# Kernel optimization log

Measured on AMD Instinct MI355X. Metric: run time of the kernel, lower is better.

The kernel has to match this reference:

```python
import jax, jax.numpy as jnp
import numpy as np

N = 50000
E = 800000
IN_DIM = 128
OUT_DIM = 128
FEAT_DIM = 64  # dstfeat_fc is nn.Linear(64, out_dim) in the source


def setup_inputs() -> dict:
    key = jax.random.key(0)
    k = jax.random.split(key, 6)
    h = jax.random.normal(k[0], (N, IN_DIM), dtype=jnp.float32)
    feat = jax.random.normal(k[1], (N, FEAT_DIM), dtype=jnp.float32)
    W_fc = jax.random.normal(k[2], (IN_DIM, OUT_DIM), dtype=jnp.float32) / np.sqrt(IN_DIM)
    W_dst = jax.random.normal(k[3], (FEAT_DIM, OUT_DIM), dtype=jnp.float32) / np.sqrt(FEAT_DIM)
    src = jax.random.randint(k[4], (E,), 0, N, dtype=jnp.int64 if jax.config.jax_enable_x64 else jnp.int32)
    dst = jax.random.randint(k[5], (E,), 0, N, dtype=jnp.int64 if jax.config.jax_enable_x64 else jnp.int32)
    return {"h": h, "feat": feat, "W_fc": W_fc, "W_dst": W_dst, "src": src, "dst": dst}


def reference(h, feat, W_fc, W_dst, src, dst):
    # z = fc(h)  -- per-node linear (bias-free)
    z = h @ W_fc                      # [N, D]
    # dstfeat = dstfeat_fc(feat) -- computed per-edge in DGL, per-node here (same math)
    dz = feat @ W_dst                 # [N, D]
    # edge_attention: e_ij = <z_src, dstfeat_dst>
    e = jnp.sum(z[src] * dz[dst], axis=-1)          # [E]
    # reduce_func: softmax over each destination's incoming mailbox, numerically stable
    emax = jax.ops.segment_max(e, dst, num_segments=N)
    emax = jnp.where(jnp.isfinite(emax), emax, 0.0)  # nodes with no in-edges
    ex = jnp.exp(e - emax[dst])                      # [E]
    denom = jax.ops.segment_sum(ex, dst, num_segments=N)
    alpha = ex / jnp.where(denom == 0, 1.0, denom)[dst]
    # weighted sum of source messages z into destination nodes
    out = jax.ops.segment_sum(alpha[:, None] * z[src], dst, num_segments=N)  # [N, D]
    return out
```

## Files before the change

kernel.cpp:

```cpp
#include <hip/hip_runtime.h>
#include <hip/hip_fp16.h>
#include <math.h>

#define IN_DIM   128
#define OUT_DIM  128
#define FEAT_DIM 64
#define NB       64
#define EBUF     6144

typedef _Float16 h2v __attribute__((ext_vector_type(2)));

__device__ __forceinline__ float2 h2f2(unsigned u) {
    __half2 h = *reinterpret_cast<const __half2*>(&u);
    return __half22float2(h);
}
__device__ __forceinline__ unsigned f2h2(float a, float b) {
    __half2 h = __floats2half2_rn(a, b);
    return *reinterpret_cast<unsigned*>(&h);
}
__device__ __forceinline__ float dot2(unsigned a, unsigned b, float c) {
#if __has_builtin(__builtin_amdgcn_fdot2)
    return __builtin_amdgcn_fdot2(*reinterpret_cast<h2v*>(&a),
                                  *reinterpret_cast<h2v*>(&b), c, false);
#else
    float2 fa = h2f2(a), fb = h2f2(b);
    return c + fa.x * fb.x + fa.y * fb.y;
#endif
}

__global__ __launch_bounds__(256) void k_wt(const float* __restrict__ Wfc,
                                            const float* __restrict__ Wdst,
                                            unsigned* __restrict__ Wfp,
                                            unsigned* __restrict__ Wdp,
                                            unsigned* __restrict__ bcounts) {
    int idx = blockIdx.x * 256 + threadIdx.x;
    if (idx < 8192) {
        int k2 = idx >> 7, c = idx & 127;
        Wfp[idx] = f2h2(Wfc[(2 * k2) * 128 + c], Wfc[(2 * k2 + 1) * 128 + c]);
    } else if (idx < 12288) {
        int i2 = idx - 8192;
        int k2 = i2 >> 7, c = i2 & 127;
        Wdp[i2] = f2h2(Wdst[(2 * k2) * 128 + c], Wdst[(2 * k2 + 1) * 128 + c]);
    }
    if (idx < 256) bcounts[idx] = 0u;
}

__global__ __launch_bounds__(256) void k_linear(
        const float* __restrict__ h, const float* __restrict__ feat,
        const unsigned* __restrict__ Wfp, const unsigned* __restrict__ Wdp,
        unsigned short* __restrict__ z_h, unsigned short* __restrict__ dz_h,
        int N, int nbz) {
    int t  = threadIdx.x;
    int c  = t & 31;
    int j0 = t >> 5;
    int b  = blockIdx.x;
    bool do_z = (b < nbz);
    int n0 = (do_z ? b : b - nbz) * NB;

    __shared__ uint2 sh[NB * 32];

    float4 acc[8];
#pragma unroll
    for (int jj = 0; jj < 8; ++jj) acc[jj] = make_float4(0.f, 0.f, 0.f, 0.f);

    if (do_z) {
        for (int i = t; i < NB * 32; i += 256) {
            int row = i >> 5, col = i & 31;
            int n = min(n0 + row, N - 1);
            float4 v = ((const float4*)(h + (size_t)n * IN_DIM))[col];
            sh[i] = make_uint2(f2h2(v.x, v.y), f2h2(v.z, v.w));
        }
        __syncthreads();

        const uint4* Wp4 = (const uint4*)Wfp;
#pragma unroll 2
        for (int k4 = 0; k4 < 32; ++k4) {
            uint4 wA = Wp4[(size_t)(2 * k4) * 32 + c];
            uint4 wB = Wp4[(size_t)(2 * k4 + 1) * 32 + c];
#pragma unroll
            for (int jj = 0; jj < 8; ++jj) {
                uint2 q = sh[(j0 * 8 + jj) * 32 + k4];
                acc[jj].x = dot2(q.y, wB.x, dot2(q.x, wA.x, acc[jj].x));
                acc[jj].y = dot2(q.y, wB.y, dot2(q.x, wA.y, acc[jj].y));
                acc[jj].z = dot2(q.y, wB.z, dot2(q.x, wA.z, acc[jj].z));
                acc[jj].w = dot2(q.y, wB.w, dot2(q.x, wA.w, acc[jj].w));
            }
        }
#pragma unroll
        for (int jj = 0; jj < 8; ++jj) {
            int n = n0 + j0 * 8 + jj;
            if (n < N) {
                uint2 pk = make_uint2(f2h2(acc[jj].x, acc[jj].y),
                                      f2h2(acc[jj].z, acc[jj].w));
                ((uint2*)(z_h + (size_t)n * OUT_DIM))[c] = pk;
            }
        }
    } else {
        for (int i = t; i < NB * 16; i += 256) {
            int row = i >> 4, col = i & 15;
            int n = min(n0 + row, N - 1);
            float4 v = ((const float4*)(feat + (size_t)n * FEAT_DIM))[col];
            sh[i] = make_uint2(f2h2(v.x, v.y), f2h2(v.z, v.w));
        }
        __syncthreads();

        const uint4* Wd4 = (const uint4*)Wdp;
#pragma unroll 2
        for (int k4 = 0; k4 < 16; ++k4) {
            uint4 wA = Wd4[(size_t)(2 * k4) * 32 + c];
            uint4 wB = Wd4[(size_t)(2 * k4 + 1) * 32 + c];
#pragma unroll
            for (int jj = 0; jj < 8; ++jj) {
                uint2 q = sh[(j0 * 8 + jj) * 16 + k4];
                acc[jj].x = dot2(q.y, wB.x, dot2(q.x, wA.x, acc[jj].x));
                acc[jj].y = dot2(q.y, wB.y, dot2(q.x, wA.y, acc[jj].y));
                acc[jj].z = dot2(q.y, wB.z, dot2(q.x, wA.z, acc[jj].z));
                acc[jj].w = dot2(q.y, wB.w, dot2(q.x, wA.w, acc[jj].w));
            }
        }
#pragma unroll
        for (int jj = 0; jj < 8; ++jj) {
            int n = n0 + j0 * 8 + jj;
            if (n < N) {
                uint2 pk = make_uint2(f2h2(acc[jj].x, acc[jj].y),
                                      f2h2(acc[jj].z, acc[jj].w));
                ((uint2*)(dz_h + (size_t)n * OUT_DIM))[c] = pk;
            }
        }
    }
}

__global__ __launch_bounds__(256) void k_bhist(const int* __restrict__ dst,
                                               unsigned* __restrict__ bcounts,
                                               int E, int nbkt) {
    __shared__ unsigned hist[256];
    int t = threadIdx.x;
    hist[t] = 0;
    __syncthreads();
    for (int i = blockIdx.x * 256 + t; i < E; i += gridDim.x * 256)
        atomicAdd(&hist[dst[i] >> 8], 1u);
    __syncthreads();
    if (t < nbkt && hist[t]) atomicAdd(&bcounts[t], hist[t]);
}

__global__ __launch_bounds__(256) void k_bscan(const unsigned* __restrict__ bcounts,
                                               unsigned* __restrict__ bstart,
                                               unsigned* __restrict__ bcursor, int nbkt) {
    __shared__ unsigned s[256];
    int t = threadIdx.x;
    unsigned v = (t < nbkt) ? bcounts[t] : 0u;
    s[t] = v;
    __syncthreads();
    for (int off = 1; off < 256; off <<= 1) {
        unsigned u = (t >= off) ? s[t - off] : 0u;
        __syncthreads();
        s[t] += u;
        __syncthreads();
    }
    if (t < nbkt) {
        unsigned excl = s[t] - v;
        bstart[t]  = excl;
        bcursor[t] = excl;
        if (t == nbkt - 1) bstart[nbkt] = s[t];
    }
}

__global__ __launch_bounds__(256) void k_bin(
        const int* __restrict__ dst, const int* __restrict__ src,
        unsigned* __restrict__ bcursor, unsigned* __restrict__ binned,
        int E, int nbkt) {
    __shared__ unsigned hist[256];
    __shared__ unsigned base[256];
    __shared__ unsigned cur[256];
    int t = threadIdx.x;
    int per = (E + gridDim.x - 1) / gridDim.x;
    int lo = blockIdx.x * per;
    int hi = min(E, lo + per);

    hist[t] = 0;
    cur[t]  = 0;
    __syncthreads();
    for (int i = lo + t; i < hi; i += 256)
        atomicAdd(&hist[dst[i] >> 8], 1u);
    __syncthreads();
    if (t < nbkt && hist[t]) base[t] = atomicAdd(&bcursor[t], hist[t]);
    __syncthreads();
    for (int i = lo + t; i < hi; i += 256) {
        int d = dst[i];
        int bk = d >> 8;
        unsigned slot = base[bk] + atomicAdd(&cur[bk], 1u);
        binned[slot] = (unsigned)src[i] | ((unsigned)(d & 255) << 24);
    }
}

__global__ __launch_bounds__(256) void k_sortx(
        const unsigned* __restrict__ binned, const unsigned* __restrict__ bstart,
        unsigned* __restrict__ offsets, unsigned* __restrict__ csr,
        int N, int E, int nbkt) {
    __shared__ unsigned ebuf[EBUF];
    __shared__ unsigned lhist[256];
    __shared__ unsigned loffx[256];
    __shared__ unsigned lcur[256];
    int b = blockIdx.x, t = threadIdx.x;
    unsigned lo = bstart[b], hi = bstart[b + 1];
    int cnt = (int)(hi - lo);
    int d0 = b << 8;
    int nd = min(N - d0, 256);
    bool fits = (cnt <= EBUF);

    lhist[t] = 0;
    lcur[t]  = 0;
    __syncthreads();

    if (fits) {
        for (int i = t; i < cnt; i += 256) {
            unsigned e = binned[lo + i];
            ebuf[i] = e;
            atomicAdd(&lhist[e >> 24], 1u);
        }
    } else {
        for (int i = t; i < cnt; i += 256)
            atomicAdd(&lhist[binned[lo + i] >> 24], 1u);
    }
    __syncthreads();

    unsigned v = lhist[t];
    loffx[t] = v;
    __syncthreads();
    for (int off = 1; off < 256; off <<= 1) {
        unsigned u = (t >= off) ? loffx[t - off] : 0u;
        __syncthreads();
        loffx[t] += u;
        __syncthreads();
    }
    unsigned excl = loffx[t] - v;
    __syncthreads();
    loffx[t] = excl;
    __syncthreads();

    if (t < nd) offsets[d0 + t] = lo + excl;
    if (b == nbkt - 1 && t == 0) offsets[N] = (unsigned)E;

    if (fits) {
        for (int i = t; i < cnt; i += 256) {
            unsigned e = ebuf[i];
            int ld = (int)(e >> 24);
            unsigned pos = loffx[ld] + atomicAdd(&lcur[ld], 1u);
            csr[lo + pos] = e & 0xFFFFFFu;
        }
    } else {
        for (int i = t; i < cnt; i += 256) {
            unsigned e = binned[lo + i];
            int ld = (int)(e >> 24);
            unsigned pos = loffx[ld] + atomicAdd(&lcur[ld], 1u);
            csr[lo + pos] = e & 0xFFFFFFu;
        }
    }
}

__global__ __launch_bounds__(256) void k_node(
        const unsigned short* __restrict__ z_h, const unsigned short* __restrict__ dz_h,
        const unsigned* __restrict__ offsets, const unsigned* __restrict__ csr,
        float* __restrict__ out, int N) {
    int lane = threadIdx.x & 63;
    int wv   = threadIdx.x >> 6;
    int g    = lane >> 4;
    int l16  = lane & 15;
    int n = blockIdx.x * 4 + wv;
    if (n >= N) return;

    unsigned start = offsets[n];
    int deg = (int)(offsets[n + 1] - start);
    float4* orow = (float4*)(out + (size_t)n * OUT_DIM);
    if (deg == 0) {
        if (g == 0) {
            orow[2 * l16]     = make_float4(0.f, 0.f, 0.f, 0.f);
            orow[2 * l16 + 1] = make_float4(0.f, 0.f, 0.f, 0.f);
        }
        return;
    }

    uint4 dq = ((const uint4*)(dz_h + (size_t)n * OUT_DIM))[l16];

    float a[8];
#pragma unroll
    for (int k = 0; k < 8; ++k) a[k] = 0.f;
    float denom = 0.f;

    for (int i = 0; i < deg; i += 8) {
        int eA = i + g;
        int eB = i + 4 + g;
        bool vA = eA < deg;
        bool vB = eB < deg;
        int sA = vA ? (int)csr[start + eA] : 0;
        int sB = vB ? (int)csr[start + eB] : 0;
        uint4 qA = ((const uint4*)(z_h + (size_t)sA * OUT_DIM))[l16];
        uint4 qB = ((const uint4*)(z_h + (size_t)sB * OUT_DIM))[l16];

        float pA = dot2(qA.w, dq.w, dot2(qA.z, dq.z, dot2(qA.y, dq.y, dot2(qA.x, dq.x, 0.f))));
        float pB = dot2(qB.w, dq.w, dot2(qB.z, dq.z, dot2(qB.y, dq.y, dot2(qB.x, dq.x, 0.f))));
#pragma unroll
        for (int off = 1; off <= 8; off <<= 1) {
            pA += __shfl_xor(pA, off);
            pB += __shfl_xor(pB, off);
        }
        float wA = vA ? __expf(pA) : 0.f;
        float wB = vB ? __expf(pB) : 0.f;
        denom += wA + wB;

        float2 zA01 = h2f2(qA.x), zA23 = h2f2(qA.y), zA45 = h2f2(qA.z), zA67 = h2f2(qA.w);
        float2 zB01 = h2f2(qB.x), zB23 = h2f2(qB.y), zB45 = h2f2(qB.z), zB67 = h2f2(qB.w);
        a[0] += wA * zA01.x + wB * zB01.x;  a[1] += wA * zA01.y + wB * zB01.y;
        a[2] += wA * zA23.x + wB * zB23.x;  a[3] += wA * zA23.y + wB * zB23.y;
        a[4] += wA * zA45.x + wB * zB45.x;  a[5] += wA * zA45.y + wB * zB45.y;
        a[6] += wA * zA67.x + wB * zB67.x;  a[7] += wA * zA67.y + wB * zB67.y;
    }

#pragma unroll
    for (int off = 16; off <= 32; off <<= 1) {
#pragma unroll
        for (int k = 0; k < 8; ++k) a[k] += __shfl_xor(a[k], off);
        denom += __shfl_xor(denom, off);
    }

    if (g == 0) {
        float inv = 1.f / denom;
        orow[2 * l16]     = make_float4(a[0] * inv, a[1] * inv, a[2] * inv, a[3] * inv);
        orow[2 * l16 + 1] = make_float4(a[4] * inv, a[5] * inv, a[6] * inv, a[7] * inv);
    }
}

extern "C" void kernel_launch(void* const* d_in, const int* in_sizes, int n_in,
                              void* d_out, int out_size, void* d_ws, size_t ws_size,
                              hipStream_t stream) {
    const float* h    = (const float*)d_in[0];
    const float* feat = (const float*)d_in[1];
    const float* Wfc  = (const float*)d_in[2];
    const float* Wdst = (const float*)d_in[3];
    const int*   src  = (const int*)d_in[4];
    const int*   dst  = (const int*)d_in[5];
    float*       out  = (float*)d_out;

    int N = in_sizes[0] / IN_DIM;
    int E = in_sizes[4];

    char* ws = (char*)d_ws;
    unsigned short* z_h  = (unsigned short*)ws; ws += (size_t)N * OUT_DIM * sizeof(unsigned short);
    unsigned short* dz_h = (unsigned short*)ws; ws += (size_t)N * OUT_DIM * sizeof(unsigned short);
    unsigned* Wfp      = (unsigned*)ws; ws += (size_t)8192 * sizeof(unsigned);
    unsigned* Wdp      = (unsigned*)ws; ws += (size_t)4096 * sizeof(unsigned);
    unsigned* binned   = (unsigned*)ws; ws += (size_t)E * sizeof(unsigned);
    unsigned* bcounts  = (unsigned*)ws; ws += (size_t)256 * sizeof(unsigned);
    unsigned* bstart   = (unsigned*)ws; ws += (size_t)260 * sizeof(unsigned);
    unsigned* bcursor  = (unsigned*)ws; ws += (size_t)256 * sizeof(unsigned);
    unsigned* offsets  = (unsigned*)ws; ws += (size_t)(N + 1) * sizeof(unsigned);
    unsigned* csr      = (unsigned*)ws;

    int nbz  = (N + NB - 1) / NB;
    int nbkt = (N + 255) / 256;

    k_wt     <<<48, 256, 0, stream>>>(Wfc, Wdst, Wfp, Wdp, bcounts);
    k_linear <<<2 * nbz, 256, 0, stream>>>(h, feat, Wfp, Wdp, z_h, dz_h, N, nbz);
    k_bhist  <<<512, 256, 0, stream>>>(dst, bcounts, E, nbkt);
    k_bscan  <<<1, 256, 0, stream>>>(bcounts, bstart, bcursor, nbkt);
    k_bin    <<<512, 256, 0, stream>>>(dst, src, bcursor, binned, E, nbkt);
    k_sortx  <<<nbkt, 256, 0, stream>>>(binned, bstart, offsets, csr, N, E, nbkt);
    k_node   <<<(N + 3) / 4, 256, 0, stream>>>(z_h, dz_h, offsets, csr, out, N);
}
```

Before: 123.4 us.

## Fold histogram into linear kernel and recompute bucket scan per block

```diff
diff --git a/kernel.cpp b/kernel.cpp
--- a/kernel.cpp
+++ b/kernel.cpp
@@ -6,6 +6,7 @@
 #define OUT_DIM  128
 #define FEAT_DIM 64
 #define NB       64
+#define NHB      512
 #define EBUF     6144
 
 typedef _Float16 h2v __attribute__((ext_vector_type(2)));
@@ -32,7 +33,7 @@
                                             const float* __restrict__ Wdst,
                                             unsigned* __restrict__ Wfp,
                                             unsigned* __restrict__ Wdp,
-                                            unsigned* __restrict__ bcounts) {
+                                            unsigned* __restrict__ bzero) {
     int idx = blockIdx.x * 256 + threadIdx.x;
     if (idx < 8192) {
         int k2 = idx >> 7, c = idx & 127;
@@ -42,22 +43,36 @@
         int k2 = i2 >> 7, c = i2 & 127;
         Wdp[i2] = f2h2(Wdst[(2 * k2) * 128 + c], Wdst[(2 * k2 + 1) * 128 + c]);
     }
-    if (idx < 256) bcounts[idx] = 0u;
-}
-
-__global__ __launch_bounds__(256) void k_linear(
+    if (idx < 512) bzero[idx] = 0u;
+}
+
+__global__ __launch_bounds__(256) void k_fused(
         const float* __restrict__ h, const float* __restrict__ feat,
         const unsigned* __restrict__ Wfp, const unsigned* __restrict__ Wdp,
         unsigned short* __restrict__ z_h, unsigned short* __restrict__ dz_h,
-        int N, int nbz) {
+        int N, int nbz,
+        const int* __restrict__ dst, unsigned* __restrict__ bcounts, int E, int nbkt) {
     int t  = threadIdx.x;
+    int b  = blockIdx.x;
+
+    __shared__ uint2 sh[NB * 32];
+
+    if (b >= 2 * nbz) {
+        unsigned* hist = (unsigned*)sh;
+        int hb = b - 2 * nbz;
+        hist[t] = 0;
+        __syncthreads();
+        for (int i = hb * 256 + t; i < E; i += NHB * 256)
+            atomicAdd(&hist[dst[i] >> 8], 1u);
+        __syncthreads();
+        if (t < nbkt && hist[t]) atomicAdd(&bcounts[t], hist[t]);
+        return;
+    }
+
     int c  = t & 31;
     int j0 = t >> 5;
-    int b  = blockIdx.x;
     bool do_z = (b < nbz);
     int n0 = (do_z ? b : b - nbz) * NB;
-
-    __shared__ uint2 sh[NB * 32];
 
     float4 acc[8];
 #pragma unroll
@@ -130,60 +145,40 @@
     }
 }
 
-__global__ __launch_bounds__(256) void k_bhist(const int* __restrict__ dst,
-                                               unsigned* __restrict__ bcounts,
-                                               int E, int nbkt) {
-    __shared__ unsigned hist[256];
-    int t = threadIdx.x;
-    hist[t] = 0;
-    __syncthreads();
-    for (int i = blockIdx.x * 256 + t; i < E; i += gridDim.x * 256)
-        atomicAdd(&hist[dst[i] >> 8], 1u);
-    __syncthreads();
-    if (t < nbkt && hist[t]) atomicAdd(&bcounts[t], hist[t]);
-}
-
-__global__ __launch_bounds__(256) void k_bscan(const unsigned* __restrict__ bcounts,
-                                               unsigned* __restrict__ bstart,
-                                               unsigned* __restrict__ bcursor, int nbkt) {
-    __shared__ unsigned s[256];
-    int t = threadIdx.x;
-    unsigned v = (t < nbkt) ? bcounts[t] : 0u;
-    s[t] = v;
-    __syncthreads();
-    for (int off = 1; off < 256; off <<= 1) {
-        unsigned u = (t >= off) ? s[t - off] : 0u;
-        __syncthreads();
-        s[t] += u;
-        __syncthreads();
-    }
-    if (t < nbkt) {
-        unsigned excl = s[t] - v;
-        bstart[t]  = excl;
-        bcursor[t] = excl;
-        if (t == nbkt - 1) bstart[nbkt] = s[t];
-    }
-}
-
 __global__ __launch_bounds__(256) void k_bin(
         const int* __restrict__ dst, const int* __restrict__ src,
-        unsigned* __restrict__ bcursor, unsigned* __restrict__ binned,
-        int E, int nbkt) {
+        const unsigned* __restrict__ bcounts, unsigned* __restrict__ breserve,
+        unsigned* __restrict__ binned, int E, int nbkt) {
+    __shared__ unsigned bst[256];
     __shared__ unsigned hist[256];
     __shared__ unsigned base[256];
     __shared__ unsigned cur[256];
     int t = threadIdx.x;
+
+    unsigned v = (t < nbkt) ? bcounts[t] : 0u;
+    bst[t] = v;
+    __syncthreads();
+    for (int off = 1; off < 256; off <<= 1) {
+        unsigned u = (t >= off) ? bst[t - off] : 0u;
+        __syncthreads();
+        bst[t] += u;
+        __syncthreads();
+    }
+    unsigned excl = bst[t] - v;
+    __syncthreads();
+    bst[t] = excl;
+    hist[t] = 0;
+    cur[t]  = 0;
+    __syncthreads();
+
     int per = (E + gridDim.x - 1) / gridDim.x;
     int lo = blockIdx.x * per;
     int hi = min(E, lo + per);
 
-    hist[t] = 0;
-    cur[t]  = 0;
-    __syncthreads();
     for (int i = lo + t; i < hi; i += 256)
         atomicAdd(&hist[dst[i] >> 8], 1u);
     __syncthreads();
-    if (t < nbkt && hist[t]) base[t] = atomicAdd(&bcursor[t], hist[t]);
+    if (t < nbkt && hist[t]) base[t] = bst[t] + atomicAdd(&breserve[t], hist[t]);
     __syncthreads();
     for (int i = lo + t; i < hi; i += 256) {
         int d = dst[i];
@@ -194,23 +189,37 @@
 }
 
 __global__ __launch_bounds__(256) void k_sortx(
-        const unsigned* __restrict__ binned, const unsigned* __restrict__ bstart,
+        const unsigned* __restrict__ binned, const unsigned* __restrict__ bcounts,
         unsigned* __restrict__ offsets, unsigned* __restrict__ csr,
         int N, int E, int nbkt) {
     __shared__ unsigned ebuf[EBUF];
+    __shared__ unsigned bst[256];
     __shared__ unsigned lhist[256];
     __shared__ unsigned loffx[256];
     __shared__ unsigned lcur[256];
     int b = blockIdx.x, t = threadIdx.x;
-    unsigned lo = bstart[b], hi = bstart[b + 1];
-    int cnt = (int)(hi - lo);
+
+    unsigned v = (t < nbkt) ? bcounts[t] : 0u;
+    bst[t] = v;
+    __syncthreads();
+    for (int off = 1; off < 256; off <<= 1) {
+        unsigned u = (t >= off) ? bst[t - off] : 0u;
+        __syncthreads();
+        bst[t] += u;
+        __syncthreads();
+    }
+    unsigned excl = bst[t] - v;
+    __syncthreads();
+    bst[t] = excl;
+    lhist[t] = 0;
+    lcur[t]  = 0;
+    __syncthreads();
+
+    unsigned lo = bst[b];
+    int cnt = (int)((b < nbkt) ? bcounts[b] : 0u);
     int d0 = b << 8;
     int nd = min(N - d0, 256);
     bool fits = (cnt <= EBUF);
-
-    lhist[t] = 0;
-    lcur[t]  = 0;
-    __syncthreads();
 
     if (fits) {
         for (int i = t; i < cnt; i += 256) {
@@ -224,8 +233,8 @@
     }
     __syncthreads();
 
-    unsigned v = lhist[t];
-    loffx[t] = v;
+    unsigned lv = lhist[t];
+    loffx[t] = lv;
     __syncthreads();
     for (int off = 1; off < 256; off <<= 1) {
         unsigned u = (t >= off) ? loffx[t - off] : 0u;
@@ -233,12 +242,12 @@
         loffx[t] += u;
         __syncthreads();
     }
-    unsigned excl = loffx[t] - v;
-    __syncthreads();
-    loffx[t] = excl;
-    __syncthreads();
-
-    if (t < nd) offsets[d0 + t] = lo + excl;
+    unsigned lexcl = loffx[t] - lv;
+    __syncthreads();
+    loffx[t] = lexcl;
+    __syncthreads();
+
+    if (t < nd) offsets[d0 + t] = lo + lexcl;
     if (b == nbkt - 1 && t == 0) offsets[N] = (unsigned)E;
 
     if (fits) {
@@ -351,19 +360,17 @@
     unsigned* Wdp      = (unsigned*)ws; ws += (size_t)4096 * sizeof(unsigned);
     unsigned* binned   = (unsigned*)ws; ws += (size_t)E * sizeof(unsigned);
     unsigned* bcounts  = (unsigned*)ws; ws += (size_t)256 * sizeof(unsigned);
-    unsigned* bstart   = (unsigned*)ws; ws += (size_t)260 * sizeof(unsigned);
-    unsigned* bcursor  = (unsigned*)ws; ws += (size_t)256 * sizeof(unsigned);
+    unsigned* breserve = (unsigned*)ws; ws += (size_t)256 * sizeof(unsigned);
     unsigned* offsets  = (unsigned*)ws; ws += (size_t)(N + 1) * sizeof(unsigned);
     unsigned* csr      = (unsigned*)ws;
 
     int nbz  = (N + NB - 1) / NB;
     int nbkt = (N + 255) / 256;
 
-    k_wt     <<<48, 256, 0, stream>>>(Wfc, Wdst, Wfp, Wdp, bcounts);
-    k_linear <<<2 * nbz, 256, 0, stream>>>(h, feat, Wfp, Wdp, z_h, dz_h, N, nbz);
-    k_bhist  <<<512, 256, 0, stream>>>(dst, bcounts, E, nbkt);
-    k_bscan  <<<1, 256, 0, stream>>>(bcounts, bstart, bcursor, nbkt);
-    k_bin    <<<512, 256, 0, stream>>>(dst, src, bcursor, binned, E, nbkt);
-    k_sortx  <<<nbkt, 256, 0, stream>>>(binned, bstart, offsets, csr, N, E, nbkt);
-    k_node   <<<(N + 3) / 4, 256, 0, stream>>>(z_h, dz_h, offsets, csr, out, N);
-}
+    k_wt    <<<48, 256, 0, stream>>>(Wfc, Wdst, Wfp, Wdp, bcounts);
+    k_fused <<<2 * nbz + NHB, 256, 0, stream>>>(h, feat, Wfp, Wdp, z_h, dz_h,
+                                                N, nbz, dst, bcounts, E, nbkt);
+    k_bin   <<<512, 256, 0, stream>>>(dst, src, bcounts, breserve, binned, E, nbkt);
+    k_sortx <<<nbkt, 256, 0, stream>>>(binned, bcounts, offsets, csr, N, E, nbkt);
+    k_node  <<<(N + 3) / 4, 256, 0, stream>>>(z_h, dz_h, offsets, csr, out, N);
+}
```

Result: faster. 111.9 us (-9.3%).
